# Optimization experiments

Measured on AMD Instinct MI355X. Metric: run time of the kernel, lower is better.

## Reference

```python
import jax, jax.numpy as jnp
import numpy as np

HIDDEN = 1024
HEADS = 16
HEAD = HIDDEN // HEADS  # 64, rotary_emb_dim == head dim
B = 8
S = 1024  # max_seqlen; all sequences full length
WINDOW = (64, 64)  # sliding_window=128 -> (64, 64)
ROPE_BASE = 10000.0


def _rope_cos_sin(seqlen, dim, base):
    inv_freq = 1.0 / (base ** (jnp.arange(0, dim, 2, dtype=jnp.float32) / dim))
    t = jnp.arange(seqlen, dtype=jnp.float32)
    freqs = jnp.outer(t, inv_freq)  # [S, dim/2]
    return jnp.cos(freqs), jnp.sin(freqs)


def _apply_rope(x, cos, sin):
    # x: [B, S, H, D], non-interleaved rotary over full head dim
    d2 = cos.shape[-1]
    x1, x2 = x[..., :d2], x[..., d2:]
    c = cos[None, :, None, :]
    s = sin[None, :, None, :]
    return jnp.concatenate([x1 * c - x2 * s, x2 * c + x1 * s], axis=-1)


def setup_inputs() -> dict:
    key = jax.random.key(0)
    k1, k2, k3 = jax.random.split(key, 3)
    hidden_states = jax.random.normal(k1, (B * S, HIDDEN), dtype=jnp.float32)
    cu_seqlens = jnp.arange(B + 1, dtype=jnp.int32) * S
    indices = jnp.arange(B * S, dtype=jnp.int32)
    attn_mask = jnp.ones((B, S), dtype=jnp.int32)
    Wqkv = jax.random.normal(k2, (3 * HIDDEN, HIDDEN), dtype=jnp.float32) * 0.02
    Wo = jax.random.normal(k3, (HIDDEN, HIDDEN), dtype=jnp.float32) * 0.02
    return {
        'hidden_states': hidden_states,
        'cu_seqlens': cu_seqlens,
        'max_seqlen': S,
        'indices': indices,
        'attn_mask': attn_mask,
        'Wqkv': Wqkv,
        'Wo': Wo,
    }


def reference(hidden_states, cu_seqlens, max_seqlen, indices, attn_mask, Wqkv, Wo):
    # QKV projection on unpadded tokens: [T, 3*H*D]
    qkv = hidden_states @ Wqkv.T
    qkv = qkv.reshape(B, S, 3, HEADS, HEAD)
    # Rotary positions reset per sequence; all sequences are full length S.
    cos, sin = _rope_cos_sin(S, HEAD, ROPE_BASE)
    q = _apply_rope(qkv[:, :, 0], cos, sin)
    k = _apply_rope(qkv[:, :, 1], cos, sin)
    v = qkv[:, :, 2]
    scores = jnp.einsum('bshd,bthd->bhst', q, k) / jnp.sqrt(jnp.float32(HEAD))
    # sliding-window mask: key j visible to query i iff i-left <= j <= i+right
    i = jnp.arange(S)[:, None]
    j = jnp.arange(S)[None, :]
    win = (j >= i - WINDOW[0]) & (j <= i + WINDOW[1])  # [S, S]
    key_mask = attn_mask.astype(bool)[:, None, None, :]  # [B,1,1,S]
    mask = win[None, None, :, :] & key_mask
    scores = jnp.where(mask, scores, jnp.finfo(scores.dtype).min)
    probs = jax.nn.softmax(scores, axis=-1)
    attn = jnp.einsum('bhst,bthd->bshd', probs, v).reshape(B * S, HIDDEN)
    return attn @ Wo.T
```

## Files before the change

kernel.cpp:

```cpp
#include <hip/hip_runtime.h>


typedef __attribute__((ext_vector_type(8))) short short8;
typedef __attribute__((ext_vector_type(4))) float f32x4;

#define SEQ   1024
#define NHEAD 16
#define HEADD 64
#define NTOK  8192

__device__ __forceinline__ unsigned short f2bf(float x) {
  unsigned u = __float_as_uint(x);
  u += 0x7fffu + ((u >> 16) & 1u);
  return (unsigned short)(u >> 16);
}

__device__ __forceinline__ void gload_lds16(const void* g, void* l) {
  __builtin_amdgcn_global_load_lds((__attribute__((address_space(1))) void*)(g),
                                   (__attribute__((address_space(3))) void*)(l),
                                   16, 0, 0);
}

__global__ __launch_bounds__(256) void prep(
    const float* __restrict__ hidden, const float* __restrict__ Wqkv,
    const float* __restrict__ Wo,
    unsigned short* __restrict__ hb, unsigned short* __restrict__ wqb,
    unsigned short* __restrict__ wob, float2* __restrict__ tab) {
  int bid = blockIdx.x;
  const float* in; unsigned short* out; int i;
  if (bid < 8192)       { in = hidden; out = hb;  i = bid * 256 + threadIdx.x; }
  else if (bid < 11264) { in = Wqkv;   out = wqb; i = (bid - 8192) * 256 + threadIdx.x; }
  else if (bid < 12288) { in = Wo;     out = wob; i = (bid - 11264) * 256 + threadIdx.x; }
  else {
    int j = (bid - 12288) * 256 + threadIdx.x;
    int s = j >> 5, d = j & 31;
    float inv = exp2f(-(float)d * 0.41524101186092034f);
    float sn, cs;
    sincosf((float)s * inv, &sn, &cs);
    tab[j] = make_float2(cs, sn);
    return;
  }
  float4 v = ((const float4*)in)[i];
  ushort4 o;
  o.x = f2bf(v.x); o.y = f2bf(v.y); o.z = f2bf(v.z); o.w = f2bf(v.w);
  ((ushort4*)out)[i] = o;
}

__global__ __launch_bounds__(256) void gemm_qkv_rope(
    const unsigned short* __restrict__ A,
    const unsigned short* __restrict__ W,
    const float2* __restrict__ tab,
    unsigned short* __restrict__ qb,
    unsigned short* __restrict__ kb,
    unsigned short* __restrict__ vt)
{
  __shared__ unsigned short As[2][128 * 64];
  __shared__ unsigned short Bs[2][128 * 64];
  const int tid  = threadIdx.x;
  const int wave = tid >> 6, lane = tid & 63;
  const int quad = lane >> 4, l15 = lane & 15;
  const int bid  = blockIdx.x;
  const int xcd  = bid & 7, idx = bid >> 3;
  const int rb   = xcd * 8 + (idx & 7);
  const int cb   = idx >> 3;
  const int row0 = rb * 128;
  const int col0 = cb * 128;
  const int mrow = (wave >> 1) * 64;
  const int ncol = (wave & 1) * 64;
  const int l7x8 = (l15 & 7) * 8;

  f32x4 acc[4][4];
#pragma unroll
  for (int i = 0; i < 4; i++)
#pragma unroll
    for (int j = 0; j < 4; j++) acc[i][j] = (f32x4){0.f, 0.f, 0.f, 0.f};

  auto stage = [&](int bi, int k0) {
#pragma unroll
    for (int i = 0; i < 4; i++) {
      int p = i * 256 + tid;
      int r = p >> 3, c = p & 7;
      int cs = c ^ (r & 7);
      gload_lds16(A + (size_t)(row0 + r) * 1024 + k0 + cs * 8, &As[bi][p * 8]);
      gload_lds16(W + (size_t)(col0 + r) * 1024 + k0 + cs * 8, &Bs[bi][p * 8]);
    }
  };

  stage(0, 0);
  __syncthreads();
  int buf = 0;
  for (int k0 = 0; k0 < 1024; k0 += 64) {
    if (k0 + 64 < 1024) stage(buf ^ 1, k0 + 64);
#pragma unroll
    for (int kk = 0; kk < 2; kk++) {
      const int qs8 = ((kk * 4 + quad) * 8) ^ l7x8;
      short8 af[4], bfr[4];
#pragma unroll
      for (int mt = 0; mt < 4; mt++)
        af[mt] = *(const short8*)&As[buf][(mrow + mt * 16 + l15) * 64 + qs8];
#pragma unroll
      for (int nt = 0; nt < 4; nt++)
        bfr[nt] = *(const short8*)&Bs[buf][(ncol + nt * 16 + l15) * 64 + qs8];
#pragma unroll
      for (int mt = 0; mt < 4; mt++)
#pragma unroll
        for (int nt = 0; nt < 4; nt++)
          acc[mt][nt] = __builtin_amdgcn_mfma_f32_16x16x32_bf16(af[mt], bfr[nt],
                                                                acc[mt][nt], 0, 0, 0);
    }
    __syncthreads();
    buf ^= 1;
  }

  const int colw  = col0 + ncol;
  const int which = colw >> 10;
  const int h     = (colw >> 6) & 15;
  const int rowg  = row0 + mrow;

  if (which == 2) {
#pragma unroll
    for (int mt = 0; mt < 4; mt++) {
      int rbase = rowg + mt * 16 + quad * 4;
      int b = rbase >> 10, s = rbase & 1023;
#pragma unroll
      for (int c = 0; c < 4; c++) {
        int d = c * 16 + l15;
        ushort4 o;
        o.x = f2bf(acc[mt][c][0]); o.y = f2bf(acc[mt][c][1]);
        o.z = f2bf(acc[mt][c][2]); o.w = f2bf(acc[mt][c][3]);
        *(ushort4*)&vt[((size_t)((b * 16 + h) * 64 + d)) * 1024 + s] = o;
      }
    }
  } else {
    unsigned short* dst = (which == 0) ? qb : kb;
    const float scale = (which == 0) ? 0.125f : 1.0f;
#pragma unroll
    for (int mt = 0; mt < 4; mt++) {
#pragma unroll
      for (int r = 0; r < 4; r++) {
        int row = rowg + mt * 16 + quad * 4 + r;
        int b = row >> 10, s = row & 1023;
        size_t base = (size_t)((b * 16 + h) * 1024 + s) * 64;
        float2 t0 = tab[s * 32 + l15];
        float2 t1 = tab[s * 32 + 16 + l15];
        float x1a = acc[mt][0][r], x2a = acc[mt][2][r];
        float x1b = acc[mt][1][r], x2b = acc[mt][3][r];
        dst[base + l15]           = f2bf((x1a * t0.x - x2a * t0.y) * scale);
        dst[base + 32 + l15]      = f2bf((x2a * t0.x + x1a * t0.y) * scale);
        dst[base + 16 + l15]      = f2bf((x1b * t1.x - x2b * t1.y) * scale);
        dst[base + 48 + l15]      = f2bf((x2b * t1.x + x1b * t1.y) * scale);
      }
    }
  }
}

__global__ __launch_bounds__(256) void attn_win(
    const unsigned short* __restrict__ qb,
    const unsigned short* __restrict__ kb,
    const unsigned short* __restrict__ vt,
    const int* __restrict__ am,
    unsigned short* __restrict__ ob)
{
  __shared__ unsigned short Ks[192 * 68];
  __shared__ unsigned short Vs[64 * 196];
  __shared__ unsigned short smask[192];

  const int tid  = threadIdx.x;
  const int wave = tid >> 6, lane = tid & 63;
  const int quad = lane >> 4, l15 = lane & 15;
  const int b  = blockIdx.x >> 4, h = blockIdx.x & 15;
  const int qs = blockIdx.y * 64;
  const size_t hb = (size_t)(b * 16 + h);
  const unsigned short* Qg = qb + hb * SEQ * 64;
  const unsigned short* Kg = kb + hb * SEQ * 64;
  const unsigned short* Vg = vt + hb * 64 * SEQ;
  const int t0 = qs - 64;

#pragma unroll
  for (int i = 0; i < 6; i++) {
    int p = i * 256 + tid;
    int r = p >> 3, c = p & 7;
    int t = t0 + r; t = t < 0 ? 0 : (t > 1023 ? 1023 : t);
    *(short8*)&Ks[r * 68 + c * 8] = *(const short8*)&Kg[(size_t)t * 64 + c * 8];
  }
  short8 vreg[6]; int vdst[6];
#pragma unroll
  for (int i = 0; i < 6; i++) {
    int p = i * 256 + tid;
    int d = p / 24, c = p % 24;
    int t = t0 + c * 8; t = t < 0 ? 0 : (t > 1016 ? 1016 : t);
    vreg[i] = *(const short8*)&Vg[(size_t)d * SEQ + t];
    vdst[i] = d * 196 + c * 8;
  }
  if (tid < 192) {
    int t = t0 + tid;
    smask[tid] = (t >= 0 && t < SEQ) ? (unsigned short)(am[b * SEQ + t] != 0) : 0;
  }
  __syncthreads();

  const int qw = qs + wave * 16;
  short8 qf0 = *(const short8*)&Qg[(size_t)(qw + l15) * 64 + quad * 8];
  short8 qf1 = *(const short8*)&Qg[(size_t)(qw + l15) * 64 + 32 + quad * 8];

  f32x4 sc[12];
#pragma unroll
  for (int tt = 0; tt < 12; tt++) {
    short8 b0 = *(const short8*)&Ks[(tt * 16 + l15) * 68 + quad * 8];
    short8 b1 = *(const short8*)&Ks[(tt * 16 + l15) * 68 + 32 + quad * 8];
    f32x4 a = (f32x4){0.f, 0.f, 0.f, 0.f};
    a = __builtin_amdgcn_mfma_f32_16x16x32_bf16(qf0, b0, a, 0, 0, 0);
    a = __builtin_amdgcn_mfma_f32_16x16x32_bf16(qf1, b1, a, 0, 0, 0);
    sc[tt] = a;
  }

  float lrow[4];
#pragma unroll
  for (int r = 0; r < 4; r++) {
    int i = qw + quad * 4 + r;
    float sum = 0.f;
#pragma unroll
    for (int tt = 0; tt < 12; tt++) {
      int t = t0 + tt * 16 + l15;
      bool ok = (t >= i - 64) && (t <= i + 64) && smask[tt * 16 + l15];
      float p = ok ? __expf(sc[tt][r]) : 0.f;
      sc[tt][r] = p;
      sum += p;
    }
#pragma unroll
    for (int off = 1; off < 16; off <<= 1) sum += __shfl_xor(sum, off);
    lrow[r] = sum;
  }

  __syncthreads();
#pragma unroll
  for (int i = 0; i < 6; i++)
    *(short8*)&Vs[vdst[i]] = vreg[i];
  unsigned short* Pw = &Ks[wave * (16 * 196)];
#pragma unroll
  for (int tt = 0; tt < 12; tt++)
#pragma unroll
    for (int r = 0; r < 4; r++)
      Pw[(quad * 4 + r) * 196 + tt * 16 + l15] = f2bf(sc[tt][r]);
  __syncthreads();

  f32x4 o[4];
#pragma unroll
  for (int dt = 0; dt < 4; dt++) o[dt] = (f32x4){0.f, 0.f, 0.f, 0.f};
#pragma unroll
  for (int kt = 0; kt < 6; kt++) {
    short8 pf = *(const short8*)&Pw[l15 * 196 + kt * 32 + quad * 8];
#pragma unroll
    for (int dt = 0; dt < 4; dt++) {
      short8 vf = *(const short8*)&Vs[(dt * 16 + l15) * 196 + kt * 32 + quad * 8];
      o[dt] = __builtin_amdgcn_mfma_f32_16x16x32_bf16(pf, vf, o[dt], 0, 0, 0);
    }
  }

#pragma unroll
  for (int r = 0; r < 4; r++) {
    float inv = 1.f / lrow[r];
    int tok = b * SEQ + qw + quad * 4 + r;
    size_t base = (size_t)tok * 1024 + h * 64;
#pragma unroll
    for (int dt = 0; dt < 4; dt++)
      ob[base + dt * 16 + l15] = f2bf(o[dt][r] * inv);
  }
}

__global__ __launch_bounds__(256) void gemm_out(
    const unsigned short* __restrict__ A,
    const unsigned short* __restrict__ W,
    float* __restrict__ out)
{
  __shared__ unsigned short As[2][128 * 64];
  __shared__ unsigned short Bs[2][128 * 64];
  const int tid  = threadIdx.x;
  const int wave = tid >> 6, lane = tid & 63;
  const int quad = lane >> 4, l15 = lane & 15;
  const int bid  = blockIdx.x;
  const int xcd  = bid & 7, idx = bid >> 3;
  const int row0 = (xcd * 8 + (idx & 7)) * 128;
  const int col0 = (idx >> 3) * 128;
  const int mrow = (wave >> 1) * 64;
  const int ncol = (wave & 1) * 64;
  const int l7x8 = (l15 & 7) * 8;

  f32x4 acc[4][4];
#pragma unroll
  for (int i = 0; i < 4; i++)
#pragma unroll
    for (int j = 0; j < 4; j++) acc[i][j] = (f32x4){0.f, 0.f, 0.f, 0.f};

  auto stage = [&](int bi, int k0) {
#pragma unroll
    for (int i = 0; i < 4; i++) {
      int p = i * 256 + tid;
      int r = p >> 3, c = p & 7;
      int cs = c ^ (r & 7);
      gload_lds16(A + (size_t)(row0 + r) * 1024 + k0 + cs * 8, &As[bi][p * 8]);
      gload_lds16(W + (size_t)(col0 + r) * 1024 + k0 + cs * 8, &Bs[bi][p * 8]);
    }
  };

  stage(0, 0);
  __syncthreads();
  int buf = 0;
  for (int k0 = 0; k0 < 1024; k0 += 64) {
    if (k0 + 64 < 1024) stage(buf ^ 1, k0 + 64);
#pragma unroll
    for (int kk = 0; kk < 2; kk++) {
      const int qs8 = ((kk * 4 + quad) * 8) ^ l7x8;
      short8 af[4], bfr[4];
#pragma unroll
      for (int mt = 0; mt < 4; mt++)
        af[mt] = *(const short8*)&As[buf][(mrow + mt * 16 + l15) * 64 + qs8];
#pragma unroll
      for (int nt = 0; nt < 4; nt++)
        bfr[nt] = *(const short8*)&Bs[buf][(ncol + nt * 16 + l15) * 64 + qs8];
#pragma unroll
      for (int mt = 0; mt < 4; mt++)
#pragma unroll
        for (int nt = 0; nt < 4; nt++)
          acc[mt][nt] = __builtin_amdgcn_mfma_f32_16x16x32_bf16(af[mt], bfr[nt],
                                                                acc[mt][nt], 0, 0, 0);
    }
    __syncthreads();
    buf ^= 1;
  }

  const int colw = col0 + ncol;
  const int rowg = row0 + mrow;
#pragma unroll
  for (int mt = 0; mt < 4; mt++)
#pragma unroll
    for (int r = 0; r < 4; r++) {
      int row = rowg + mt * 16 + quad * 4 + r;
#pragma unroll
      for (int nt = 0; nt < 4; nt++)
        out[(size_t)row * 1024 + colw + nt * 16 + l15] = acc[mt][nt][r];
    }
}

extern "C" void kernel_launch(void* const* d_in, const int* in_sizes, int n_in,
                              void* d_out, int out_size, void* d_ws, size_t ws_size,
                              hipStream_t stream) {
  const float* hidden = (const float*)d_in[0];
  const int*   am     = (const int*)d_in[4];
  const float* Wqkv   = (const float*)d_in[5];
  const float* Wo     = (const float*)d_in[6];
  float* out = (float*)d_out;

  char* ws = (char*)d_ws;
  unsigned short* hb  = (unsigned short*)(ws);
  unsigned short* wqb = (unsigned short*)(ws + (size_t)(16 << 20));
  unsigned short* wob = (unsigned short*)(ws + (size_t)(22 << 20));
  unsigned short* qbf = (unsigned short*)(ws + (size_t)(24 << 20));
  unsigned short* kbf = (unsigned short*)(ws + (size_t)(40 << 20));
  unsigned short* vtb = (unsigned short*)(ws + (size_t)(56 << 20));
  float2*         tab = (float2*)(ws + (size_t)(72 << 20));
  unsigned short* ab  = hb;

  prep<<<12416, 256, 0, stream>>>(hidden, Wqkv, Wo, hb, wqb, wob, tab);

  gemm_qkv_rope<<<1536, 256, 0, stream>>>(hb, wqb, tab, qbf, kbf, vtb);

  dim3 g2(128, 16);
  attn_win<<<g2, 256, 0, stream>>>(qbf, kbf, vtb, am, ab);

  gemm_out<<<512, 256, 0, stream>>>(ab, wob, out);
}
```

Measured before the change: 217.2 us.

## Deepen QKV GEMM pipeline to four-stage K=32 buffers with explicit vmcnt waits

Changes the QKV projection GEMM from a two-buffer K=64 loop to a four-buffer K=32 ring, keeping three tile loads in flight ahead of compute. Explicit vmcnt waits and raw barriers replace the full __syncthreads, and global addresses are precomputed once. A new XOR swizzle matches the 32-wide rows. The goal is to hide global-to-LDS latency behind the MFMAs. The cost is more barriers per unit of K and fewer MFMAs per barrier.

Result: slower. 233.8 us (+7.6%).

```diff
diff --git a/kernel.cpp b/kernel.cpp
--- a/kernel.cpp
+++ b/kernel.cpp
@@ -54,8 +54,8 @@
     unsigned short* __restrict__ kb,
     unsigned short* __restrict__ vt)
 {
-  __shared__ unsigned short As[2][128 * 64];
-  __shared__ unsigned short Bs[2][128 * 64];
+  __shared__ unsigned short As[4][128 * 32];
+  __shared__ unsigned short Bs[4][128 * 32];
   const int tid  = threadIdx.x;
   const int wave = tid >> 6, lane = tid & 63;
   const int quad = lane >> 4, l15 = lane & 15;
@@ -67,7 +67,15 @@
   const int col0 = cb * 128;
   const int mrow = (wave >> 1) * 64;
   const int ncol = (wave & 1) * 64;
-  const int l7x8 = (l15 & 7) * 8;
+  const int qs8  = (quad ^ ((l15 >> 1) & 3)) * 8;
+
+  const int p0 = tid, p1 = tid + 256;
+  const int r0 = p0 >> 2, cs0 = (p0 & 3) ^ ((r0 >> 1) & 3);
+  const int r1 = p1 >> 2, cs1 = (p1 & 3) ^ ((r1 >> 1) & 3);
+  const unsigned short* ga0 = A + (size_t)(row0 + r0) * 1024 + cs0 * 8;
+  const unsigned short* ga1 = A + (size_t)(row0 + r1) * 1024 + cs1 * 8;
+  const unsigned short* gb0 = W + (size_t)(col0 + r0) * 1024 + cs0 * 8;
+  const unsigned short* gb1 = W + (size_t)(col0 + r1) * 1024 + cs1 * 8;
 
   f32x4 acc[4][4];
 #pragma unroll
@@ -75,41 +83,46 @@
 #pragma unroll
     for (int j = 0; j < 4; j++) acc[i][j] = (f32x4){0.f, 0.f, 0.f, 0.f};
 
-  auto stage = [&](int bi, int k0) {
-#pragma unroll
-    for (int i = 0; i < 4; i++) {
-      int p = i * 256 + tid;
-      int r = p >> 3, c = p & 7;
-      int cs = c ^ (r & 7);
-      gload_lds16(A + (size_t)(row0 + r) * 1024 + k0 + cs * 8, &As[bi][p * 8]);
-      gload_lds16(W + (size_t)(col0 + r) * 1024 + k0 + cs * 8, &Bs[bi][p * 8]);
-    }
+  auto stage = [&](int bi, int koff) {
+    gload_lds16(ga0 + koff, &As[bi][p0 * 8]);
+    gload_lds16(ga1 + koff, &As[bi][p1 * 8]);
+    gload_lds16(gb0 + koff, &Bs[bi][p0 * 8]);
+    gload_lds16(gb1 + koff, &Bs[bi][p1 * 8]);
   };
 
-  stage(0, 0);
-  __syncthreads();
-  int buf = 0;
-  for (int k0 = 0; k0 < 1024; k0 += 64) {
-    if (k0 + 64 < 1024) stage(buf ^ 1, k0 + 64);
-#pragma unroll
-    for (int kk = 0; kk < 2; kk++) {
-      const int qs8 = ((kk * 4 + quad) * 8) ^ l7x8;
-      short8 af[4], bfr[4];
-#pragma unroll
-      for (int mt = 0; mt < 4; mt++)
-        af[mt] = *(const short8*)&As[buf][(mrow + mt * 16 + l15) * 64 + qs8];
+  stage(0, 0); stage(1, 32); stage(2, 64);
+
+#pragma unroll 1
+  for (int t = 0; t < 32; ++t) {
+    if (t < 29) {
+      stage((t + 3) & 3, (t + 3) * 32);
+      asm volatile("s_waitcnt vmcnt(12)" ::: "memory");
+    } else if (t == 29) {
+      asm volatile("s_waitcnt vmcnt(8)" ::: "memory");
+    } else if (t == 30) {
+      asm volatile("s_waitcnt vmcnt(4)" ::: "memory");
+    } else {
+      asm volatile("s_waitcnt vmcnt(0)" ::: "memory");
+    }
+    __builtin_amdgcn_s_barrier();
+
+    const int bi = t & 3;
+    short8 af[4], bfr[4];
+#pragma unroll
+    for (int mt = 0; mt < 4; mt++)
+      af[mt] = *(const short8*)&As[bi][(mrow + mt * 16 + l15) * 32 + qs8];
+#pragma unroll
+    for (int nt = 0; nt < 4; nt++)
+      bfr[nt] = *(const short8*)&Bs[bi][(ncol + nt * 16 + l15) * 32 + qs8];
+    asm volatile("s_waitcnt lgkmcnt(0)" ::: "memory");
+    __builtin_amdgcn_sched_barrier(0);
+    __builtin_amdgcn_s_barrier();
+#pragma unroll
+    for (int mt = 0; mt < 4; mt++)
 #pragma unroll
       for (int nt = 0; nt < 4; nt++)
-        bfr[nt] = *(const short8*)&Bs[buf][(ncol + nt * 16 + l15) * 64 + qs8];
-#pragma unroll
-      for (int mt = 0; mt < 4; mt++)
-#pragma unroll
-        for (int nt = 0; nt < 4; nt++)
-          acc[mt][nt] = __builtin_amdgcn_mfma_f32_16x16x32_bf16(af[mt], bfr[nt],
-                                                                acc[mt][nt], 0, 0, 0);
-    }
-    __syncthreads();
-    buf ^= 1;
+        acc[mt][nt] = __builtin_amdgcn_mfma_f32_16x16x32_bf16(af[mt], bfr[nt],
+                                                              acc[mt][nt], 0, 0, 0);
   }
 
   const int colw  = col0 + ncol;
```

## Widen attention blocks to 128 queries and trim per-wave key tiles to the window

Applied to the files above, without the earlier changes.

Each attention block now handles 128 queries with 8 waves over a shared 256-key K/V tile. The larger tile reduces the redundant halo loads of K and V per query, and each wave computes only the 9 key tiles (144 keys) that can overlap its sliding window instead of all 12. The PV product runs over 160 keys, zero-padded, using a per-wave offset into V. In exchange, shared memory per block grows and the block size doubles, which may lower occupancy, and the padding and offset indexing must be exactly right for correctness.

Result: faster. 208.7 us (-3.9%).

```diff
diff --git a/kernel.cpp b/kernel.cpp
--- a/kernel.cpp
+++ b/kernel.cpp
@@ -154,22 +154,22 @@
   }
 }
 
-__global__ __launch_bounds__(256) void attn_win(
+__global__ __launch_bounds__(512) void attn_win(
     const unsigned short* __restrict__ qb,
     const unsigned short* __restrict__ kb,
     const unsigned short* __restrict__ vt,
     const int* __restrict__ am,
     unsigned short* __restrict__ ob)
 {
-  __shared__ unsigned short Ks[192 * 68];
-  __shared__ unsigned short Vs[64 * 196];
-  __shared__ unsigned short smask[192];
+  __shared__ unsigned short KP[20992];
+  __shared__ unsigned short Vs[64 * 260];
+  __shared__ unsigned short smask[256];
 
   const int tid  = threadIdx.x;
   const int wave = tid >> 6, lane = tid & 63;
   const int quad = lane >> 4, l15 = lane & 15;
   const int b  = blockIdx.x >> 4, h = blockIdx.x & 15;
-  const int qs = blockIdx.y * 64;
+  const int qs = blockIdx.y * 128;
   const size_t hb = (size_t)(b * 16 + h);
   const unsigned short* Qg = qb + hb * SEQ * 64;
   const unsigned short* Kg = kb + hb * SEQ * 64;
@@ -177,22 +177,26 @@
   const int t0 = qs - 64;
 
 #pragma unroll
-  for (int i = 0; i < 6; i++) {
-    int p = i * 256 + tid;
+  for (int i = 0; i < 4; i++) {
+    int p = i * 512 + tid;
     int r = p >> 3, c = p & 7;
     int t = t0 + r; t = t < 0 ? 0 : (t > 1023 ? 1023 : t);
-    *(short8*)&Ks[r * 68 + c * 8] = *(const short8*)&Kg[(size_t)t * 64 + c * 8];
-  }
-  short8 vreg[6]; int vdst[6];
-#pragma unroll
-  for (int i = 0; i < 6; i++) {
-    int p = i * 256 + tid;
-    int d = p / 24, c = p % 24;
+    *(short8*)&KP[r * 68 + c * 8] = *(const short8*)&Kg[(size_t)t * 64 + c * 8];
+  }
+  short8 vreg[4]; int vdst[4];
+#pragma unroll
+  for (int i = 0; i < 4; i++) {
+    int p = i * 512 + tid;
+    int d = p >> 5, c = p & 31;
     int t = t0 + c * 8; t = t < 0 ? 0 : (t > 1016 ? 1016 : t);
     vreg[i] = *(const short8*)&Vg[(size_t)d * SEQ + t];
-    vdst[i] = d * 196 + c * 8;
-  }
-  if (tid < 192) {
+    vdst[i] = d * 260 + c * 8;
+  }
+  if (tid < 64) {
+    Vs[tid * 260 + 256] = 0; Vs[tid * 260 + 257] = 0;
+    Vs[tid * 260 + 258] = 0; Vs[tid * 260 + 259] = 0;
+  }
+  if (tid < 256) {
     int t = t0 + tid;
     smask[tid] = (t >= 0 && t < SEQ) ? (unsigned short)(am[b * SEQ + t] != 0) : 0;
   }
@@ -202,15 +206,16 @@
   short8 qf0 = *(const short8*)&Qg[(size_t)(qw + l15) * 64 + quad * 8];
   short8 qf1 = *(const short8*)&Qg[(size_t)(qw + l15) * 64 + 32 + quad * 8];
 
-  f32x4 sc[12];
-#pragma unroll
-  for (int tt = 0; tt < 12; tt++) {
-    short8 b0 = *(const short8*)&Ks[(tt * 16 + l15) * 68 + quad * 8];
-    short8 b1 = *(const short8*)&Ks[(tt * 16 + l15) * 68 + 32 + quad * 8];
+  f32x4 sc[9];
+#pragma unroll
+  for (int tt2 = 0; tt2 < 9; tt2++) {
+    int kr = (wave + tt2) * 16 + l15;
+    short8 b0 = *(const short8*)&KP[kr * 68 + quad * 8];
+    short8 b1 = *(const short8*)&KP[kr * 68 + 32 + quad * 8];
     f32x4 a = (f32x4){0.f, 0.f, 0.f, 0.f};
     a = __builtin_amdgcn_mfma_f32_16x16x32_bf16(qf0, b0, a, 0, 0, 0);
     a = __builtin_amdgcn_mfma_f32_16x16x32_bf16(qf1, b1, a, 0, 0, 0);
-    sc[tt] = a;
+    sc[tt2] = a;
   }
 
   float lrow[4];
@@ -219,11 +224,12 @@
     int i = qw + quad * 4 + r;
     float sum = 0.f;
 #pragma unroll
-    for (int tt = 0; tt < 12; tt++) {
-      int t = t0 + tt * 16 + l15;
-      bool ok = (t >= i - 64) && (t <= i + 64) && smask[tt * 16 + l15];
-      float p = ok ? __expf(sc[tt][r]) : 0.f;
-      sc[tt][r] = p;
+    for (int tt2 = 0; tt2 < 9; tt2++) {
+      int kl = (wave + tt2) * 16 + l15;
+      int t = t0 + kl;
+      bool ok = (t >= i - 64) && (t <= i + 64) && smask[kl];
+      float p = ok ? __expf(sc[tt2][r]) : 0.f;
+      sc[tt2][r] = p;
       sum += p;
     }
 #pragma unroll
@@ -233,25 +239,29 @@
 
   __syncthreads();
 #pragma unroll
-  for (int i = 0; i < 6; i++)
+  for (int i = 0; i < 4; i++)
     *(short8*)&Vs[vdst[i]] = vreg[i];
-  unsigned short* Pw = &Ks[wave * (16 * 196)];
-#pragma unroll
-  for (int tt = 0; tt < 12; tt++)
+  unsigned short* Pw = &KP[wave * (16 * 164)];
+#pragma unroll
+  for (int tt2 = 0; tt2 < 9; tt2++)
 #pragma unroll
     for (int r = 0; r < 4; r++)
-      Pw[(quad * 4 + r) * 196 + tt * 16 + l15] = f2bf(sc[tt][r]);
+      Pw[(quad * 4 + r) * 164 + tt2 * 16 + l15] = f2bf(sc[tt2][r]);
+#pragma unroll
+  for (int r = 0; r < 4; r++)
+    Pw[(quad * 4 + r) * 164 + 144 + l15] = 0;
   __syncthreads();
 
   f32x4 o[4];
 #pragma unroll
   for (int dt = 0; dt < 4; dt++) o[dt] = (f32x4){0.f, 0.f, 0.f, 0.f};
 #pragma unroll
-  for (int kt = 0; kt < 6; kt++) {
-    short8 pf = *(const short8*)&Pw[l15 * 196 + kt * 32 + quad * 8];
+  for (int kt = 0; kt < 5; kt++) {
+    short8 pf = *(const short8*)&Pw[l15 * 164 + kt * 32 + quad * 8];
 #pragma unroll
     for (int dt = 0; dt < 4; dt++) {
-      short8 vf = *(const short8*)&Vs[(dt * 16 + l15) * 196 + kt * 32 + quad * 8];
+      short8 vf = *(const short8*)&Vs[(dt * 16 + l15) * 260 +
+                                      wave * 16 + kt * 32 + quad * 8];
       o[dt] = __builtin_amdgcn_mfma_f32_16x16x32_bf16(pf, vf, o[dt], 0, 0, 0);
     }
   }
@@ -364,8 +374,8 @@
 
   gemm_qkv_rope<<<1536, 256, 0, stream>>>(hb, wqb, tab, qbf, kbf, vtb);
 
-  dim3 g2(128, 16);
-  attn_win<<<g2, 256, 0, stream>>>(qbf, kbf, vtb, am, ab);
+  dim3 g2(128, 8);
+  attn_win<<<g2, 512, 0, stream>>>(qbf, kbf, vtb, am, ab);
 
   gemm_out<<<512, 256, 0, stream>>>(ab, wob, out);
 }
```
